# Performance work log

Hardware: AMD Instinct MI355X
Metric: run time of the kernel (lower is better)

Reference implementation:

```python
import jax, jax.numpy as jnp
import numpy as np


def setup_inputs() -> dict:
    key = jax.random.key(0)
    k1, k2 = jax.random.split(key)
    x = jax.random.normal(k1, (32, 16, 256, 256), dtype=jnp.float32)
    weight = jax.random.normal(k2, (5, 5), dtype=jnp.float32)
    return {"input": x, "weight": weight}


def reference(input, weight):
    # Original: per-(n,m) FFT-based 'full' 2D convolution with a shared 5x5 kernel.
    # Full linear convolution == correlation with the flipped kernel and (p-1, q-1) padding.
    a, b, c, d = input.shape
    p, q = weight.shape
    x = input.reshape(a * b, 1, c, d)                 # fold (batch, channel) into batch; 1 feature channel
    w = weight[::-1, ::-1].reshape(1, 1, p, q)        # flip kernel: lax conv is cross-correlation
    out = jax.lax.conv_general_dilated(
        x, w,
        window_strides=(1, 1),
        padding=((p - 1, p - 1), (q - 1, q - 1)),     # 'full' convolution
        dimension_numbers=("NCHW", "OIHW", "NCHW"),
    )
    return out.reshape(a, b, c + p - 1, d + q - 1)
```

## Files before the change

### kernel.cpp

```cpp
#include <hip/hip_runtime.h>


#define IMG 256
#define OW  260
#define TXN 65
#define NIMG 512
#define TOTAL (NIMG * OW * TXN)

__global__ __launch_bounds__(256) void conv_full_kernel(
    const float* __restrict__ in, const float* __restrict__ w,
    float* __restrict__ out)
{
    float wt[25];
#pragma unroll
    for (int i = 0; i < 25; ++i) wt[i] = w[i];

    int idx = blockIdx.x * 256 + threadIdx.x;
    if (idx >= TOTAL) return;

    int tx4 = idx % TXN;
    int t   = idx / TXN;
    int y   = t % OW;
    int n   = t / OW;
    int x0  = tx4 * 4;

    const float* img = in + (size_t)n * IMG * IMG;

    int xl = x0 - 4; if (xl < 0) xl = 0;
    int xh = x0;     if (xh > IMG - 4) xh = IMG - 4;
    const bool zL = (tx4 == 0);
    const bool zR = (tx4 == TXN - 1);

    float acc0 = 0.f, acc1 = 0.f, acc2 = 0.f, acc3 = 0.f;

#pragma unroll
    for (int a = 0; a < 5; ++a) {
        int yy = y - a;
        if (yy >= 0 && yy < IMG) {
            const float* rb = img + yy * IMG;
            float4 lo = *(const float4*)(rb + xl);
            float4 hi = *(const float4*)(rb + xh);
            float v[8];
            v[0] = zL ? 0.f : lo.x;
            v[1] = zL ? 0.f : lo.y;
            v[2] = zL ? 0.f : lo.z;
            v[3] = zL ? 0.f : lo.w;
            v[4] = zR ? 0.f : hi.x;
            v[5] = zR ? 0.f : hi.y;
            v[6] = zR ? 0.f : hi.z;
            v[7] = zR ? 0.f : hi.w;
#pragma unroll
            for (int b = 0; b < 5; ++b) {
                float wv = wt[a * 5 + b];
                acc0 = fmaf(v[4 - b], wv, acc0);
                acc1 = fmaf(v[5 - b], wv, acc1);
                acc2 = fmaf(v[6 - b], wv, acc2);
                acc3 = fmaf(v[7 - b], wv, acc3);
            }
        }
    }

    float4 o = make_float4(acc0, acc1, acc2, acc3);
    *(float4*)(out + (size_t)idx * 4) = o;
}

extern "C" void kernel_launch(void* const* d_in, const int* in_sizes, int n_in,
                              void* d_out, int out_size, void* d_ws, size_t ws_size,
                              hipStream_t stream) {
    const float* in = (const float*)d_in[0];
    const float* w  = (const float*)d_in[1];
    float* out = (float*)d_out;

    int blocks = (TOTAL + 255) / 256;
    conv_full_kernel<<<blocks, 256, 0, stream>>>(in, w, out);
}
```

Baseline: 251.2 us.

## Process 10-row vertical strips per thread with a rolling 5-row register window

Each thread now computes a 4-wide column over 10 consecutive output rows instead of a single row. It keeps a rolling window of 5 input rows in registers, so each input row is loaded once per strip rather than five times. This cuts redundant global and L2 loads and per-thread setup overhead. In exchange there are fewer threads, more registers per thread, and serialized row work inside each thread. The bounds check is dropped because the thread count divides exactly by 256.

```diff
diff --git a/kernel.cpp b/kernel.cpp
--- a/kernel.cpp
+++ b/kernel.cpp
@@ -4,10 +4,12 @@
 #define IMG 256
 #define OW  260
 #define TXN 65
+#define ROWS 10
+#define STRIPS 26
 #define NIMG 512
-#define TOTAL (NIMG * OW * TXN)
+#define NTHREADS (NIMG * STRIPS * TXN)
 
-__global__ __launch_bounds__(256) void conv_full_kernel(
+__global__ __launch_bounds__(256) void conv_full_strip(
     const float* __restrict__ in, const float* __restrict__ w,
     float* __restrict__ out)
 {
@@ -16,52 +18,69 @@
     for (int i = 0; i < 25; ++i) wt[i] = w[i];
 
     int idx = blockIdx.x * 256 + threadIdx.x;
-    if (idx >= TOTAL) return;
-
     int tx4 = idx % TXN;
     int t   = idx / TXN;
-    int y   = t % OW;
-    int n   = t / OW;
+    int s   = t % STRIPS;
+    int n   = t / STRIPS;
+    int y0  = s * ROWS;
     int x0  = tx4 * 4;
-
-    const float* img = in + (size_t)n * IMG * IMG;
 
     int xl = x0 - 4; if (xl < 0) xl = 0;
     int xh = x0;     if (xh > IMG - 4) xh = IMG - 4;
     const bool zL = (tx4 == 0);
     const bool zR = (tx4 == TXN - 1);
 
-    float acc0 = 0.f, acc1 = 0.f, acc2 = 0.f, acc3 = 0.f;
+    const float* img  = in + (size_t)n * IMG * IMG;
+    float*       outp = out + (((size_t)n * OW + y0) * TXN + tx4) * 4;
+
+    float win[5][8];
+
+#define LOAD_ROW(slot, yy)                                          \
+    do {                                                            \
+        int _yy = (yy);                                             \
+        if (_yy >= 0 && _yy < IMG) {                                \
+            const float* _rb = img + _yy * IMG;                     \
+            float4 _lo = *(const float4*)(_rb + xl);                \
+            float4 _hi = *(const float4*)(_rb + xh);                \
+            win[slot][0] = zL ? 0.f : _lo.x;                        \
+            win[slot][1] = zL ? 0.f : _lo.y;                        \
+            win[slot][2] = zL ? 0.f : _lo.z;                        \
+            win[slot][3] = zL ? 0.f : _lo.w;                        \
+            win[slot][4] = zR ? 0.f : _hi.x;                        \
+            win[slot][5] = zR ? 0.f : _hi.y;                        \
+            win[slot][6] = zR ? 0.f : _hi.z;                        \
+            win[slot][7] = zR ? 0.f : _hi.w;                        \
+        } else {                                                    \
+            _Pragma("unroll")                                       \
+            for (int _i = 0; _i < 8; ++_i) win[slot][_i] = 0.f;     \
+        }                                                           \
+    } while (0)
+
+    LOAD_ROW(0, y0 - 4);
+    LOAD_ROW(1, y0 - 3);
+    LOAD_ROW(2, y0 - 2);
+    LOAD_ROW(3, y0 - 1);
 
 #pragma unroll
-    for (int a = 0; a < 5; ++a) {
-        int yy = y - a;
-        if (yy >= 0 && yy < IMG) {
-            const float* rb = img + yy * IMG;
-            float4 lo = *(const float4*)(rb + xl);
-            float4 hi = *(const float4*)(rb + xh);
-            float v[8];
-            v[0] = zL ? 0.f : lo.x;
-            v[1] = zL ? 0.f : lo.y;
-            v[2] = zL ? 0.f : lo.z;
-            v[3] = zL ? 0.f : lo.w;
-            v[4] = zR ? 0.f : hi.x;
-            v[5] = zR ? 0.f : hi.y;
-            v[6] = zR ? 0.f : hi.z;
-            v[7] = zR ? 0.f : hi.w;
+    for (int r = 0; r < ROWS; ++r) {
+        LOAD_ROW((4 + r) % 5, y0 + r);
+
+        float acc0 = 0.f, acc1 = 0.f, acc2 = 0.f, acc3 = 0.f;
+#pragma unroll
+        for (int a = 0; a < 5; ++a) {
+            const float* vv = win[(4 + r - a) % 5];
 #pragma unroll
             for (int b = 0; b < 5; ++b) {
                 float wv = wt[a * 5 + b];
-                acc0 = fmaf(v[4 - b], wv, acc0);
-                acc1 = fmaf(v[5 - b], wv, acc1);
-                acc2 = fmaf(v[6 - b], wv, acc2);
-                acc3 = fmaf(v[7 - b], wv, acc3);
+                acc0 = fmaf(vv[4 - b], wv, acc0);
+                acc1 = fmaf(vv[5 - b], wv, acc1);
+                acc2 = fmaf(vv[6 - b], wv, acc2);
+                acc3 = fmaf(vv[7 - b], wv, acc3);
             }
         }
+        *(float4*)(outp + r * (TXN * 4)) = make_float4(acc0, acc1, acc2, acc3);
     }
-
-    float4 o = make_float4(acc0, acc1, acc2, acc3);
-    *(float4*)(out + (size_t)idx * 4) = o;
+#undef LOAD_ROW
 }
 
 extern "C" void kernel_launch(void* const* d_in, const int* in_sizes, int n_in,
@@ -71,6 +90,6 @@
     const float* w  = (const float*)d_in[1];
     float* out = (float*)d_out;
 
-    int blocks = (TOTAL + 255) / 256;
-    conv_full_kernel<<<blocks, 256, 0, stream>>>(in, w, out);
+    int blocks = NTHREADS / 256;
+    conv_full_strip<<<blocks, 256, 0, stream>>>(in, w, out);
 }
```

After: 258.0 us. 1.03x slower.
